# Performance work log

Measured on AMD Instinct MI355X. Metric: run time of the kernel, lower is better.

Reference implementation:

```python
import jax, jax.numpy as jnp
import numpy as np

TRACT_SPECS = [
    dict(name="x_a", src_size=4096, dst_size=1024, connections=64, seed=42),
    dict(name="x_b", src_size=4096, dst_size=512, connections=64, seed=43),
    dict(name="x_c", src_size=2048, dst_size=512, connections=32, seed=44),
]


def _make_mask(dst_size, src_size, n_conn, seed):
    rng = np.random.RandomState(seed)
    mask = np.zeros((dst_size, src_size), dtype=np.float32)
    for dst in range(dst_size):
        idx = rng.choice(src_size, size=min(n_conn, src_size), replace=False)
        mask[dst, idx] = 1.0
    return jnp.asarray(mask)


def _xavier_uniform(key, dst, src):
    # matches nn.init.xavier_uniform_ for a (dst, src) weight
    limit = float(np.sqrt(6.0 / (dst + src)))
    return jax.random.uniform(key, (dst, src), jnp.float32, -limit, limit)


def setup_inputs() -> dict:
    key = jax.random.key(0)
    keys = jax.random.split(key, 6)
    B, S = 8, 1024
    inp = {}
    for i, spec in enumerate(TRACT_SPECS):
        src, dst = spec["src_size"], spec["dst_size"]
        inp[spec["name"]] = jax.random.normal(keys[i], (B, S, src), jnp.float32)
        inp["w_" + spec["name"][-1]] = _xavier_uniform(keys[3 + i], dst, src)
        inp["m_" + spec["name"][-1]] = _make_mask(dst, src, spec["connections"], spec["seed"])
    return inp


def reference(x_a, x_b, x_c, w_a, w_b, w_c, m_a, m_b, m_c):
    # Each tract: F.linear(x, weight * mask) -> x @ (W*M)^T; then concat on last dim.
    out_a = jnp.einsum("bsi,oi->bso", x_a, w_a * m_a)
    out_b = jnp.einsum("bsi,oi->bso", x_b, w_b * m_b)
    out_c = jnp.einsum("bsi,oi->bso", x_c, w_c * m_c)
    return jnp.concatenate([out_a, out_b, out_c], axis=-1)
```

## Files before the change

### kernel.cpp

```cpp
#include <hip/hip_runtime.h>
#include <hip/hip_fp16.h>
#include <stdint.h>


#define BS_TOTAL 8192
#define SRC_A 4096
#define SRC_B 4096
#define SRC_C 2048
#define DST_A 1024
#define DST_B 512
#define DST_C 512
#define K_A 64
#define K_B 64
#define K_C 32
#define OUT_DIM 2048
#define ROWS 4
#define NBLK (BS_TOTAL / ROWS)
#define LDS_BYTES (SRC_A * 8)

typedef float f32x4 __attribute__((ext_vector_type(4)));


__global__ __launch_bounds__(256) void compress_kernel(
    const float* __restrict__ w_a, const float* __restrict__ m_a,
    const float* __restrict__ w_b, const float* __restrict__ m_b,
    const float* __restrict__ w_c, const float* __restrict__ m_c,
    unsigned* __restrict__ pa, unsigned* __restrict__ pb,
    unsigned* __restrict__ pc) {
    __shared__ int s_cnt;
    __shared__ int s_idx[64];
    __shared__ int s_bankcnt[16];
    __shared__ int s_bankoff[16];
    __shared__ unsigned s_sorted[64];

    const int blk = blockIdx.x;
    const int t = threadIdx.x;

    const float *w, *m;
    unsigned* p;
    int dst, src_n, K, DST;
    if (blk < DST_A) {
        w = w_a; m = m_a; p = pa; dst = blk;
        src_n = SRC_A; K = K_A; DST = DST_A;
    } else if (blk < DST_A + DST_B) {
        w = w_b; m = m_b; p = pb; dst = blk - DST_A;
        src_n = SRC_B; K = K_B; DST = DST_B;
    } else {
        w = w_c; m = m_c; p = pc; dst = blk - DST_A - DST_B;
        src_n = SRC_C; K = K_C; DST = DST_C;
    }

    if (t == 0) s_cnt = 0;
    if (t < 16) s_bankcnt[t] = 0;
    __syncthreads();

    const float* mrow = m + (size_t)dst * src_n;
    const float* wrow = w + (size_t)dst * src_n;
    const f32x4* m4 = (const f32x4*)mrow;
    const int nq = src_n >> 10;
    for (int i = 0; i < nq; ++i) {
        int q = t + (i << 8);
        f32x4 mv = m4[q];
#pragma unroll
        for (int j = 0; j < 4; ++j) {
            if (mv[j] != 0.0f) {
                int pos = atomicAdd(&s_cnt, 1);
                if (pos < 64) s_idx[pos] = 4 * q + j;
            }
        }
    }
    __syncthreads();
    int cnt = s_cnt;
    if (cnt > K) cnt = K;

    if (t < cnt) {
        int idx = s_idx[t];
        unsigned u = (unsigned)idx >> 1;
        unsigned up = u ^ ((u >> 3) & 7u);
        int key = (int)(((up & 7u) << 1) | ((unsigned)idx & 1u));
        atomicAdd(&s_bankcnt[key], 1);
    }
    __syncthreads();
    if (t == 0) {
        int acc = 0;
        for (int b = 0; b < 16; ++b) {
            s_bankoff[b] = acc;
            acc += s_bankcnt[b];
        }
    }
    __syncthreads();
    if (t < cnt) {
        int idx = s_idx[t];
        unsigned u = (unsigned)idx >> 1;
        unsigned up = u ^ ((u >> 3) & 7u);
        unsigned boff = (up << 4) | (((unsigned)idx & 1u) << 3);
        int key = (int)(((up & 7u) << 1) | ((unsigned)idx & 1u));
        int j = atomicAdd(&s_bankoff[key], 1);
        float wv = wrow[idx] * mrow[idx];
        unsigned hb = (unsigned)__half_as_ushort(__float2half(wv));
        s_sorted[j] = (boff << 16) | hb;
    }
    __syncthreads();
    if (t >= cnt && t < K) s_sorted[t] = 0u;
    __syncthreads();

    if (t < K) {
        int rot = (K == 64) ? ((dst & 15) << 2) : ((dst & 15) << 1);
        unsigned v = s_sorted[(t + rot) & (K - 1)];
        p[(((t >> 2) * DST) + dst) * 4 + (t & 3)] = v;
    }
}


#define PROC(u, A0, A1, A2, A3) {                                            \
        const uint2 xv = *(const uint2*)((const char*)xs + ((u) >> 16));     \
        const float w = __half2float(__ushort_as_half((unsigned short)((u) & 0xffffu))); \
        const __half2 hlo = *(const __half2*)&xv.x;                          \
        const __half2 hhi = *(const __half2*)&xv.y;                          \
        A0 = fmaf(w, __low2float(hlo), A0);                                  \
        A1 = fmaf(w, __high2float(hlo), A1);                                 \
        A2 = fmaf(w, __low2float(hhi), A2);                                  \
        A3 = fmaf(w, __high2float(hhi), A3); }

template <int SRCN, int KQ, int DSTN, int NPAIR>
__device__ __forceinline__ void do_tract(
    const float* __restrict__ xsrc, const uint4* __restrict__ tab,
    float* __restrict__ outb,
    size_t r0, int t, unsigned* xs) {
    const f32x4* s0 = (const f32x4*)(xsrc + (r0 + 0) * SRCN);
    const f32x4* s1 = (const f32x4*)(xsrc + (r0 + 1) * SRCN);
    const f32x4* s2 = (const f32x4*)(xsrc + (r0 + 2) * SRCN);
    const f32x4* s3 = (const f32x4*)(xsrc + (r0 + 3) * SRCN);
    uint4* xs4 = (uint4*)xs;

#pragma unroll
    for (int i = 0; i < (SRCN >> 10); ++i) {
        int q = t + (i << 8);
        f32x4 v0 = s0[q];
        f32x4 v1 = s1[q];
        f32x4 v2 = s2[q];
        f32x4 v3 = s3[q];
        uint4 w0, w1;
        __half2 h;
        h = __floats2half2_rn(v0.x, v1.x); w0.x = *(unsigned*)&h;
        h = __floats2half2_rn(v2.x, v3.x); w0.y = *(unsigned*)&h;
        h = __floats2half2_rn(v0.y, v1.y); w0.z = *(unsigned*)&h;
        h = __floats2half2_rn(v2.y, v3.y); w0.w = *(unsigned*)&h;
        h = __floats2half2_rn(v0.z, v1.z); w1.x = *(unsigned*)&h;
        h = __floats2half2_rn(v2.z, v3.z); w1.y = *(unsigned*)&h;
        h = __floats2half2_rn(v0.w, v1.w); w1.z = *(unsigned*)&h;
        h = __floats2half2_rn(v2.w, v3.w); w1.w = *(unsigned*)&h;
        unsigned u0 = (unsigned)(2 * q);
        unsigned up0 = u0 ^ ((u0 >> 3) & 7u);
        xs4[up0]     = w0;
        xs4[up0 ^ 1] = w1;
    }
    __syncthreads();

#pragma unroll 1
    for (int op = 0; op < NPAIR; ++op) {
        const int d0 = t + (op << 9);
        float a0 = 0.f, a1 = 0.f, a2 = 0.f, a3 = 0.f;
        float b0 = 0.f, b1 = 0.f, b2 = 0.f, b3 = 0.f;
#pragma unroll 4
        for (int k4 = 0; k4 < KQ; ++k4) {
            uint4 e0 = tab[k4 * DSTN + d0];
            uint4 e1 = tab[k4 * DSTN + d0 + 256];
            PROC(e0.x, a0, a1, a2, a3)
            PROC(e1.x, b0, b1, b2, b3)
            PROC(e0.y, a0, a1, a2, a3)
            PROC(e1.y, b0, b1, b2, b3)
            PROC(e0.z, a0, a1, a2, a3)
            PROC(e1.z, b0, b1, b2, b3)
            PROC(e0.w, a0, a1, a2, a3)
            PROC(e1.w, b0, b1, b2, b3)
        }
        __builtin_nontemporal_store(a0, outb + 0 * OUT_DIM + d0);
        __builtin_nontemporal_store(a1, outb + 1 * OUT_DIM + d0);
        __builtin_nontemporal_store(a2, outb + 2 * OUT_DIM + d0);
        __builtin_nontemporal_store(a3, outb + 3 * OUT_DIM + d0);
        __builtin_nontemporal_store(b0, outb + 0 * OUT_DIM + d0 + 256);
        __builtin_nontemporal_store(b1, outb + 1 * OUT_DIM + d0 + 256);
        __builtin_nontemporal_store(b2, outb + 2 * OUT_DIM + d0 + 256);
        __builtin_nontemporal_store(b3, outb + 3 * OUT_DIM + d0 + 256);
    }
}

__global__ __launch_bounds__(256) void tract_kernel(
    const float* __restrict__ x_a, const float* __restrict__ x_b,
    const float* __restrict__ x_c,
    const unsigned* __restrict__ pa, const unsigned* __restrict__ pb,
    const unsigned* __restrict__ pc,
    float* __restrict__ out) {
    extern __shared__ unsigned xs[];
    const int t = threadIdx.x;
    const int blk = blockIdx.x;

    if (blk < NBLK) {
        size_t r0 = (size_t)blk * ROWS;
        do_tract<SRC_A, K_A / 4, DST_A, 2>(
            x_a, (const uint4*)pa, out + r0 * OUT_DIM, r0, t, xs);
    } else if (blk < 2 * NBLK) {
        size_t r0 = (size_t)(blk - NBLK) * ROWS;
        do_tract<SRC_B, K_B / 4, DST_B, 1>(
            x_b, (const uint4*)pb, out + r0 * OUT_DIM + DST_A, r0, t, xs);
    } else {
        size_t r0 = (size_t)(blk - 2 * NBLK) * ROWS;
        do_tract<SRC_C, K_C / 4, DST_C, 1>(
            x_c, (const uint4*)pc, out + r0 * OUT_DIM + DST_A + DST_B, r0, t, xs);
    }
}

extern "C" void kernel_launch(void* const* d_in, const int* in_sizes, int n_in,
                              void* d_out, int out_size, void* d_ws, size_t ws_size,
                              hipStream_t stream) {
    const float* x_a = (const float*)d_in[0];
    const float* w_a = (const float*)d_in[1];
    const float* m_a = (const float*)d_in[2];
    const float* x_b = (const float*)d_in[3];
    const float* w_b = (const float*)d_in[4];
    const float* m_b = (const float*)d_in[5];
    const float* x_c = (const float*)d_in[6];
    const float* w_c = (const float*)d_in[7];
    const float* m_c = (const float*)d_in[8];
    float* out = (float*)d_out;

    char* ws = (char*)d_ws;
    unsigned* pa = (unsigned*)(ws);
    unsigned* pb = (unsigned*)(ws + 262144);
    unsigned* pc = (unsigned*)(ws + 262144 + 131072);

    compress_kernel<<<DST_A + DST_B + DST_C, 256, 0, stream>>>(
        w_a, m_a, w_b, m_b, w_c, m_c, pa, pb, pc);
    tract_kernel<<<3 * NBLK, 256, LDS_BYTES, stream>>>(
        x_a, x_b, x_c, pa, pb, pc, out);
}
```

Before: 389.9 us.

## Use 512-thread tract blocks and bank-balanced weight table packing

The tract kernel moves from 256 to 512 threads per block, so each thread handles one or two output columns instead of looping over pairs, and the LDS staging loop is halved per thread. The compress kernel now spreads nonzero entries evenly across LDS bank keys (a capped count per key, with overflow filling free slots) instead of sorting by bank, so that each group of four table entries hits distinct banks. The half-to-float weight conversion is inlined per FMA. The aim is more waves in flight and fewer LDS bank conflicts during the gather, at the cost of higher per-block resource use and possibly lower occupancy per CU.

```diff
diff --git a/kernel.cpp b/kernel.cpp
--- a/kernel.cpp
+++ b/kernel.cpp
@@ -15,6 +15,7 @@
 #define K_C 32
 #define OUT_DIM 2048
 #define ROWS 4
+#define THREADS 512
 #define NBLK (BS_TOTAL / ROWS)
 #define LDS_BYTES (SRC_A * 8)
 
@@ -29,8 +30,9 @@
     unsigned* __restrict__ pc) {
     __shared__ int s_cnt;
     __shared__ int s_idx[64];
-    __shared__ int s_bankcnt[16];
-    __shared__ int s_bankoff[16];
+    __shared__ int s_paircnt[16];
+    __shared__ int s_ovf_cnt;
+    __shared__ unsigned s_ovf[64];
     __shared__ unsigned s_sorted[64];
 
     const int blk = blockIdx.x;
@@ -49,9 +51,11 @@
         w = w_c; m = m_c; p = pc; dst = blk - DST_A - DST_B;
         src_n = SRC_C; K = K_C; DST = DST_C;
     }
-
-    if (t == 0) s_cnt = 0;
-    if (t < 16) s_bankcnt[t] = 0;
+    const int CAP = K >> 4;
+
+    if (t == 0) { s_cnt = 0; s_ovf_cnt = 0; }
+    if (t < 16) s_paircnt[t] = 0;
+    if (t < 64) s_sorted[t] = 0u;
     __syncthreads();
 
     const float* mrow = m + (size_t)dst * src_n;
@@ -77,35 +81,34 @@
         int idx = s_idx[t];
         unsigned u = (unsigned)idx >> 1;
         unsigned up = u ^ ((u >> 3) & 7u);
-        int key = (int)(((up & 7u) << 1) | ((unsigned)idx & 1u));
-        atomicAdd(&s_bankcnt[key], 1);
-    }
-    __syncthreads();
-    if (t == 0) {
-        int acc = 0;
-        for (int b = 0; b < 16; ++b) {
-            s_bankoff[b] = acc;
-            acc += s_bankcnt[b];
-        }
-    }
-    __syncthreads();
-    if (t < cnt) {
-        int idx = s_idx[t];
-        unsigned u = (unsigned)idx >> 1;
-        unsigned up = u ^ ((u >> 3) & 7u);
         unsigned boff = (up << 4) | (((unsigned)idx & 1u) << 3);
         int key = (int)(((up & 7u) << 1) | ((unsigned)idx & 1u));
-        int j = atomicAdd(&s_bankoff[key], 1);
         float wv = wrow[idx] * mrow[idx];
         unsigned hb = (unsigned)__half_as_ushort(__float2half(wv));
-        s_sorted[j] = (boff << 16) | hb;
-    }
-    __syncthreads();
-    if (t >= cnt && t < K) s_sorted[t] = 0u;
+        unsigned packed = (boff << 16) | hb;
+        int r = atomicAdd(&s_paircnt[key], 1);
+        if (r < CAP) {
+            s_sorted[key * CAP + r] = packed;
+        } else {
+            int o = atomicAdd(&s_ovf_cnt, 1);
+            s_ovf[o] = packed;
+        }
+    }
+    __syncthreads();
+    if (t == 0) {
+        int total = s_ovf_cnt;
+        int o = 0;
+        for (int b = 0; b < 16 && o < total; ++b) {
+            int fill = s_paircnt[b];
+            if (fill > CAP) fill = CAP;
+            for (int r = fill; r < CAP && o < total; ++r)
+                s_sorted[b * CAP + r] = s_ovf[o++];
+        }
+    }
     __syncthreads();
 
     if (t < K) {
-        int rot = (K == 64) ? ((dst & 15) << 2) : ((dst & 15) << 1);
+        int rot = (dst & 15) * CAP;
         unsigned v = s_sorted[(t + rot) & (K - 1)];
         p[(((t >> 2) * DST) + dst) * 4 + (t & 3)] = v;
     }
@@ -114,15 +117,15 @@
 
 #define PROC(u, A0, A1, A2, A3) {                                            \
         const uint2 xv = *(const uint2*)((const char*)xs + ((u) >> 16));     \
-        const float w = __half2float(__ushort_as_half((unsigned short)((u) & 0xffffu))); \
+        const __half wh = __ushort_as_half((unsigned short)((u) & 0xffffu)); \
         const __half2 hlo = *(const __half2*)&xv.x;                          \
         const __half2 hhi = *(const __half2*)&xv.y;                          \
-        A0 = fmaf(w, __low2float(hlo), A0);                                  \
-        A1 = fmaf(w, __high2float(hlo), A1);                                 \
-        A2 = fmaf(w, __low2float(hhi), A2);                                  \
-        A3 = fmaf(w, __high2float(hhi), A3); }
-
-template <int SRCN, int KQ, int DSTN, int NPAIR>
+        A0 = fmaf(__half2float(wh), __low2float(hlo), A0);                   \
+        A1 = fmaf(__half2float(wh), __high2float(hlo), A1);                  \
+        A2 = fmaf(__half2float(wh), __low2float(hhi), A2);                   \
+        A3 = fmaf(__half2float(wh), __high2float(hhi), A3); }
+
+template <int SRCN, int KQ, int DSTN, bool DUAL>
 __device__ __forceinline__ void do_tract(
     const float* __restrict__ xsrc, const uint4* __restrict__ tab,
     float* __restrict__ outb,
@@ -134,8 +137,8 @@
     uint4* xs4 = (uint4*)xs;
 
 #pragma unroll
-    for (int i = 0; i < (SRCN >> 10); ++i) {
-        int q = t + (i << 8);
+    for (int i = 0; i < (SRCN >> 11); ++i) {
+        int q = t + (i << 9);
         f32x4 v0 = s0[q];
         f32x4 v1 = s1[q];
         f32x4 v2 = s2[q];
@@ -157,15 +160,13 @@
     }
     __syncthreads();
 
-#pragma unroll 1
-    for (int op = 0; op < NPAIR; ++op) {
-        const int d0 = t + (op << 9);
+    if constexpr (DUAL) {
         float a0 = 0.f, a1 = 0.f, a2 = 0.f, a3 = 0.f;
         float b0 = 0.f, b1 = 0.f, b2 = 0.f, b3 = 0.f;
 #pragma unroll 4
         for (int k4 = 0; k4 < KQ; ++k4) {
-            uint4 e0 = tab[k4 * DSTN + d0];
-            uint4 e1 = tab[k4 * DSTN + d0 + 256];
+            uint4 e0 = tab[k4 * DSTN + t];
+            uint4 e1 = tab[k4 * DSTN + t + 512];
             PROC(e0.x, a0, a1, a2, a3)
             PROC(e1.x, b0, b1, b2, b3)
             PROC(e0.y, a0, a1, a2, a3)
@@ -175,18 +176,32 @@
             PROC(e0.w, a0, a1, a2, a3)
             PROC(e1.w, b0, b1, b2, b3)
         }
-        __builtin_nontemporal_store(a0, outb + 0 * OUT_DIM + d0);
-        __builtin_nontemporal_store(a1, outb + 1 * OUT_DIM + d0);
-        __builtin_nontemporal_store(a2, outb + 2 * OUT_DIM + d0);
-        __builtin_nontemporal_store(a3, outb + 3 * OUT_DIM + d0);
-        __builtin_nontemporal_store(b0, outb + 0 * OUT_DIM + d0 + 256);
-        __builtin_nontemporal_store(b1, outb + 1 * OUT_DIM + d0 + 256);
-        __builtin_nontemporal_store(b2, outb + 2 * OUT_DIM + d0 + 256);
-        __builtin_nontemporal_store(b3, outb + 3 * OUT_DIM + d0 + 256);
-    }
-}
-
-__global__ __launch_bounds__(256) void tract_kernel(
+        __builtin_nontemporal_store(a0, outb + 0 * OUT_DIM + t);
+        __builtin_nontemporal_store(a1, outb + 1 * OUT_DIM + t);
+        __builtin_nontemporal_store(a2, outb + 2 * OUT_DIM + t);
+        __builtin_nontemporal_store(a3, outb + 3 * OUT_DIM + t);
+        __builtin_nontemporal_store(b0, outb + 0 * OUT_DIM + t + 512);
+        __builtin_nontemporal_store(b1, outb + 1 * OUT_DIM + t + 512);
+        __builtin_nontemporal_store(b2, outb + 2 * OUT_DIM + t + 512);
+        __builtin_nontemporal_store(b3, outb + 3 * OUT_DIM + t + 512);
+    } else {
+        float a0 = 0.f, a1 = 0.f, a2 = 0.f, a3 = 0.f;
+#pragma unroll 4
+        for (int k4 = 0; k4 < KQ; ++k4) {
+            uint4 e0 = tab[k4 * DSTN + t];
+            PROC(e0.x, a0, a1, a2, a3)
+            PROC(e0.y, a0, a1, a2, a3)
+            PROC(e0.z, a0, a1, a2, a3)
+            PROC(e0.w, a0, a1, a2, a3)
+        }
+        __builtin_nontemporal_store(a0, outb + 0 * OUT_DIM + t);
+        __builtin_nontemporal_store(a1, outb + 1 * OUT_DIM + t);
+        __builtin_nontemporal_store(a2, outb + 2 * OUT_DIM + t);
+        __builtin_nontemporal_store(a3, outb + 3 * OUT_DIM + t);
+    }
+}
+
+__global__ __launch_bounds__(THREADS) void tract_kernel(
     const float* __restrict__ x_a, const float* __restrict__ x_b,
     const float* __restrict__ x_c,
     const unsigned* __restrict__ pa, const unsigned* __restrict__ pb,
@@ -198,15 +213,15 @@
 
     if (blk < NBLK) {
         size_t r0 = (size_t)blk * ROWS;
-        do_tract<SRC_A, K_A / 4, DST_A, 2>(
+        do_tract<SRC_A, K_A / 4, DST_A, true>(
             x_a, (const uint4*)pa, out + r0 * OUT_DIM, r0, t, xs);
     } else if (blk < 2 * NBLK) {
         size_t r0 = (size_t)(blk - NBLK) * ROWS;
-        do_tract<SRC_B, K_B / 4, DST_B, 1>(
+        do_tract<SRC_B, K_B / 4, DST_B, false>(
             x_b, (const uint4*)pb, out + r0 * OUT_DIM + DST_A, r0, t, xs);
     } else {
         size_t r0 = (size_t)(blk - 2 * NBLK) * ROWS;
-        do_tract<SRC_C, K_C / 4, DST_C, 1>(
+        do_tract<SRC_C, K_C / 4, DST_C, false>(
             x_c, (const uint4*)pc, out + r0 * OUT_DIM + DST_A + DST_B, r0, t, xs);
     }
 }
@@ -232,6 +247,6 @@
 
     compress_kernel<<<DST_A + DST_B + DST_C, 256, 0, stream>>>(
         w_a, m_a, w_b, m_b, w_c, m_c, pa, pb, pc);
-    tract_kernel<<<3 * NBLK, 256, LDS_BYTES, stream>>>(
+    tract_kernel<<<3 * NBLK, THREADS, LDS_BYTES, stream>>>(
         x_a, x_b, x_c, pa, pb, pc, out);
 }
```

Result: no change. 385.7 us (-1.1%).
